# Performance work log

Measured on AMD Instinct MI355X. Metric: run time of the kernel, lower is better.

Reference implementation:

```python
import jax, jax.numpy as jnp
import numpy as np

B, S, E = 2, 4096, 640
H, D, G = 4, 256, 1      # n_heads, head_dim, n_kv_groups
WINDOW = 512
SCALING = 256.0 ** -0.5  # query_pre_attn_scalar ** -0.5
EPS = 1e-6


def rmsnorm(x, scale):
    # Gemma variant: weight = 1 + scale, computed in fp32 over last dim
    xf = x.astype(jnp.float32)
    var = jnp.mean(xf * xf, axis=-1, keepdims=True)
    return (xf * jax.lax.rsqrt(var + EPS) * (1.0 + scale.astype(jnp.float32))).astype(x.dtype)


def apply_rope(x, cos, sin):
    # x: [B, h, S, D]; cos/sin: [S, D]
    half = x.shape[-1] // 2
    x1, x2 = x[..., :half], x[..., half:]
    rotated = jnp.concatenate([-x2, x1], axis=-1)
    return (x * cos[None, None] + rotated * sin[None, None]).astype(x.dtype)


def setup_inputs() -> dict:
    key = jax.random.key(0)
    ks = jax.random.split(key, 6)
    x = jax.random.normal(ks[0], (B, S, E), dtype=jnp.float32)
    # weights (torch Linear weight.T layout: [in, out])
    Wq = jax.random.normal(ks[1], (E, H * D), dtype=jnp.float32) * 0.02
    Wk = jax.random.normal(ks[2], (E, G * D), dtype=jnp.float32) * 0.02
    Wv = jax.random.normal(ks[3], (E, G * D), dtype=jnp.float32) * 0.02
    Wo = jax.random.normal(ks[4], (H * D, E), dtype=jnp.float32) * 0.02
    q_scale = jnp.zeros((D,), dtype=jnp.float32)
    k_scale = jnp.zeros((D,), dtype=jnp.float32)
    # RoPE tables (theta = rope_local_base = 10000 for sliding layers)
    inv_freq = 1.0 / (10000.0 ** (jnp.arange(0, D, 2, dtype=jnp.float32) / D))
    angles = jnp.arange(S, dtype=jnp.float32)[:, None] * inv_freq[None, :]
    angles = jnp.concatenate([angles, angles], axis=1)  # [S, D]
    cos, sin = jnp.cos(angles), jnp.sin(angles)
    # causal + sliding-window mask; True = masked out
    i = jnp.arange(S)[:, None]
    j = jnp.arange(S)[None, :]
    mask = (j > i) | ((i - j) >= WINDOW)
    return {"x": x, "mask": mask, "cos": cos, "sin": sin,
            "Wq": Wq, "Wk": Wk, "Wv": Wv, "Wo": Wo,
            "q_scale": q_scale, "k_scale": k_scale}


def reference(x, mask, cos, sin, Wq, Wk, Wv, Wo, q_scale, k_scale):
    b, s, _ = x.shape
    q = (x @ Wq).reshape(b, s, H, D).transpose(0, 2, 1, 3)  # [B,H,S,D]
    k = (x @ Wk).reshape(b, s, G, D).transpose(0, 2, 1, 3)  # [B,G,S,D]
    v = (x @ Wv).reshape(b, s, G, D).transpose(0, 2, 1, 3)  # [B,G,S,D]
    q = rmsnorm(q, q_scale)
    k = rmsnorm(k, k_scale)
    q = apply_rope(q, cos, sin)
    k = apply_rope(k, cos, sin)
    # GQA: K/V have G=1 heads; broadcasting replaces repeat_interleave
    scores = (q * SCALING) @ jnp.swapaxes(k, -1, -2)  # [B,H,S,S]
    scores = jnp.where(mask[None, None], -jnp.inf, scores)
    attn = jax.nn.softmax(scores, axis=-1)
    out = attn @ v                                     # [B,H,S,D]
    out = out.transpose(0, 2, 1, 3).reshape(b, s, H * D)
    return out @ Wo
```

## Files before the change

kernel.cpp:

```cpp
#include <hip/hip_runtime.h>
#include <hip/hip_bf16.h>
#include <stdint.h>

#define BB 2
#define SS 4096
#define EE 640
#define HH 4
#define DD 256
#define WIN 512

typedef __attribute__((ext_vector_type(8))) short bv8;
typedef __attribute__((ext_vector_type(4))) float fv4;
typedef __attribute__((ext_vector_type(16))) float fv16;

__device__ __forceinline__ unsigned short f2b(float f) {
  union { float f; unsigned u; } a; a.f = f;
  unsigned r = a.u + 0x7fffu + ((a.u >> 16) & 1u);
  return (unsigned short)(r >> 16);
}
__device__ __forceinline__ float b2f(unsigned short s) {
  union { unsigned u; float f; } a; a.u = ((unsigned)s) << 16;
  return a.f;
}
__device__ __forceinline__ unsigned pk2(float lo, float hi_) {
  return (unsigned)f2b(lo) | ((unsigned)f2b(hi_) << 16);
}

typedef const __attribute__((address_space(1))) unsigned int* as1u;
typedef __attribute__((address_space(3))) unsigned int* as3u;
__device__ __forceinline__ void gld16(const unsigned short* g, unsigned short* l) {
  __builtin_amdgcn_global_load_lds((as1u)(const void*)g, (as3u)(void*)l, 16, 0, 0);
}

__global__ __launch_bounds__(256) void k_cast_bf16(const float* __restrict__ src,
                                                   unsigned short* __restrict__ dst, int n4) {
  int i = blockIdx.x * 256 + threadIdx.x;
  if (i >= n4) return;
  fv4 v = ((const fv4*)src)[i];
  ushort4 o; o.x = f2b(v.x); o.y = f2b(v.y); o.z = f2b(v.z); o.w = f2b(v.w);
  ((ushort4*)dst)[i] = o;
}

template <typename T>
__global__ __launch_bounds__(256) void k_transpose_bf16(const T* __restrict__ src,
    unsigned short* __restrict__ dst, int sstride, int dstride) {
  __shared__ float tile[32][33];
  int r0 = blockIdx.x * 32, c0 = blockIdx.y * 32;
  int t = threadIdx.x;
  int rr = t >> 3, cc = (t & 7) * 4;
  const T* p = src + (size_t)(r0 + rr) * sstride + c0 + cc;
  float v[4];
  if constexpr (sizeof(T) == 4) {
    fv4 x = *(const fv4*)p;
    v[0] = x.x; v[1] = x.y; v[2] = x.z; v[3] = x.w;
  } else {
    ushort4 x = *(const ushort4*)p;
    v[0] = b2f(x.x); v[1] = b2f(x.y); v[2] = b2f(x.z); v[3] = b2f(x.w);
  }
#pragma unroll
  for (int i = 0; i < 4; ++i) tile[cc + i][rr] = v[i];
  __syncthreads();
  ushort4 o;
  o.x = f2b(tile[rr][cc + 0]); o.y = f2b(tile[rr][cc + 1]);
  o.z = f2b(tile[rr][cc + 2]); o.w = f2b(tile[rr][cc + 3]);
  *(ushort4*)(dst + (size_t)(c0 + rr) * dstride + r0 + cc) = o;
}

template <bool OUT_BF16, int BN>
__global__ __launch_bounds__(256) void k_gemm(const unsigned short* __restrict__ A,
    const unsigned short* __restrict__ Bt, void* __restrict__ Cp,
    int M, int N, int K, int nt_n) {
  __shared__ unsigned short la[128 * 32];
  __shared__ unsigned short lb[BN * 32];
  const int bid = blockIdx.x;
  const int gidx = (bid & 7) * (gridDim.x >> 3) + (bid >> 3);
  const int m0 = (gidx / nt_n) * 128, n0 = (gidx % nt_n) * BN;
  const int tid = threadIdx.x, lane = tid & 63, wave = tid >> 6;
  const int g = lane >> 4, lr = lane & 15;
  constexpr int MI = (BN == 128) ? 4 : 2;
  const int wm = (BN == 128) ? (wave >> 1) * 64 : wave * 32;
  const int wn = (BN == 128) ? (wave & 1) * 64 : 0;
  fv4 acc[MI][4] = {};
  const int srow = wave * 32 + (lane >> 2);
  const int sch = (lane & 3) * 8;
  const unsigned short* ga0 = A + (size_t)(m0 + srow) * K + sch;
  unsigned short* lad = la + wave * 1024;
  const int srowb = (BN == 128) ? srow : (wave * 16 + (lane >> 2));
  const unsigned short* gb0 = Bt + (size_t)(n0 + srowb) * K + sch;
  unsigned short* lbd = lb + ((BN == 128) ? wave * 1024 : wave * 512);
  for (int k0 = 0; k0 < K; k0 += 32) {
    __syncthreads();
    gld16(ga0 + k0, lad);
    gld16(ga0 + (size_t)16 * K + k0, lad + 512);
    gld16(gb0 + k0, lbd);
    if constexpr (BN == 128) gld16(gb0 + (size_t)16 * K + k0, lbd + 512);
    __syncthreads();
    bv8 af[MI], bf[4];
#pragma unroll
    for (int mi = 0; mi < MI; ++mi) af[mi] = *(const bv8*)(la + (wm + mi * 16 + lr) * 32 + g * 8);
#pragma unroll
    for (int ni = 0; ni < 4; ++ni) bf[ni] = *(const bv8*)(lb + (wn + ni * 16 + lr) * 32 + g * 8);
    __builtin_amdgcn_s_setprio(1);
#pragma unroll
    for (int mi = 0; mi < MI; ++mi)
#pragma unroll
      for (int ni = 0; ni < 4; ++ni)
        acc[mi][ni] = __builtin_amdgcn_mfma_f32_16x16x32_bf16(af[mi], bf[ni], acc[mi][ni], 0, 0, 0);
    __builtin_amdgcn_s_setprio(0);
  }
#pragma unroll
  for (int mi = 0; mi < MI; ++mi) {
#pragma unroll
    for (int r = 0; r < 4; ++r) {
      size_t row = (size_t)(m0 + wm + mi * 16 + g * 4 + r);
#pragma unroll
      for (int ni = 0; ni < 4; ++ni) {
        int col = n0 + wn + ni * 16 + lr;
        float val = acc[mi][ni][r];
        if constexpr (OUT_BF16)
          ((unsigned short*)Cp)[row * N + col] = f2b(val);
        else
          ((float*)Cp)[row * N + col] = val;
      }
    }
  }
}

__global__ __launch_bounds__(320) void k_normrope(const unsigned short* __restrict__ qkv,
    const float* __restrict__ cosp, const float* __restrict__ sinp,
    const float* __restrict__ qsc, const float* __restrict__ ksc,
    unsigned short* __restrict__ qo, unsigned short* __restrict__ ko) {
  int m = blockIdx.x;
  int b = m >> 12, s = m & 4095;
  int wave = threadIdx.x >> 6, lane = threadIdx.x & 63;
  bool isq = wave < 4;
  const unsigned short* src = qkv + (size_t)m * 1536 + (isq ? wave * 256 : 1024);
  const float* scp = isq ? qsc : ksc;
  int d0 = lane * 4;
  ushort4 raw = *(const ushort4*)(src + d0);
  float x0 = b2f(raw.x), x1 = b2f(raw.y), x2 = b2f(raw.z), x3 = b2f(raw.w);
  float ss = x0 * x0 + x1 * x1 + x2 * x2 + x3 * x3;
#pragma unroll
  for (int off = 1; off < 64; off <<= 1) ss += __shfl_xor(ss, off, 64);
  float rs = rsqrtf(ss * (1.0f / 256.0f) + 1e-6f);
  fv4 sc = *(const fv4*)(scp + d0);
  float n0 = x0 * rs * (1.0f + sc.x);
  float n1 = x1 * rs * (1.0f + sc.y);
  float n2 = x2 * rs * (1.0f + sc.z);
  float n3 = x3 * rs * (1.0f + sc.w);
  float p0 = __shfl_xor(n0, 32, 64);
  float p1 = __shfl_xor(n1, 32, 64);
  float p2 = __shfl_xor(n2, 32, 64);
  float p3 = __shfl_xor(n3, 32, 64);
  float sgn = (lane < 32) ? -1.0f : 1.0f;
  fv4 c4 = *(const fv4*)(cosp + (size_t)s * 256 + d0);
  fv4 s4 = *(const fv4*)(sinp + (size_t)s * 256 + d0);
  float mult = isq ? 0.0625f : 1.0f;
  float o0 = (n0 * c4.x + sgn * p0 * s4.x) * mult;
  float o1 = (n1 * c4.y + sgn * p1 * s4.y) * mult;
  float o2 = (n2 * c4.z + sgn * p2 * s4.z) * mult;
  float o3 = (n3 * c4.w + sgn * p3 * s4.w) * mult;
  ushort4 o; o.x = f2b(o0); o.y = f2b(o1); o.z = f2b(o2); o.w = f2b(o3);
  unsigned short* dst = isq
      ? qo + ((size_t)(b * HH + wave) * SS + s) * 256 + d0
      : ko + ((size_t)b * SS + s) * 256 + d0;
  *(ushort4*)dst = o;
}

__global__ __launch_bounds__(512, 2) void k_attn(const unsigned short* __restrict__ q,
    const unsigned short* __restrict__ kg, const unsigned short* __restrict__ vtg,
    unsigned short* __restrict__ att) {
  __shared__ __align__(16) char ldsbuf[133120];
  __shared__ float lsb[4][32];
  unsigned short* kt = (unsigned short*)ldsbuf;
  unsigned short* vl = (unsigned short*)ldsbuf + 32768;
  const int bid = blockIdx.x;
  const int gidx = (bid & 7) * 32 + (bid >> 3);
  const int b = gidx >> 7;
  const int i0 = (gidx & 127) * 32;
  const int tid = threadIdx.x, wave = tid >> 6, lane = tid & 63;
  const int h = wave >> 1, ks = wave & 1;
  const int hi = lane >> 5, l31 = lane & 31;
  bv8 qf[16];
  {
    const unsigned short* qp = q + ((size_t)(b * HH + h) * SS + i0 + l31) * 256;
#pragma unroll
    for (int m = 0; m < 16; ++m) qf[m] = *(const bv8*)(qp + m * 16 + hi * 8);
  }
  fv16 po[8] = {};
  float lsp = 0.f;
  const int t0 = (i0 >= WIN) ? ((i0 - WIN + 1) >> 6) : 0;
  const int t1 = i0 >> 6;
  const unsigned short* kb = kg + (size_t)b * SS * 256;
  const unsigned short* vb = vtg + (size_t)b * 256 * SS;
  auto stageK = [&](int t, int pp) {
    const unsigned short* kbase = kb + (size_t)t * 64 * 256;
    unsigned short* dst = kt + pp * 16384;
#pragma unroll
    for (int c = 0; c < 4; ++c) {
      int slot = c * 512 + tid;
      int row = slot >> 5, s = slot & 31;
      gld16(kbase + (size_t)row * 256 + ((s ^ (row & 7)) * 8),
            dst + (c * 512 + wave * 64) * 8);
    }
  };
  auto stageV = [&](int t, int pp) {
    const unsigned short* vbase = vb + (size_t)t * 64;
    unsigned short* dst = vl + pp * 16384;
#pragma unroll
    for (int c = 0; c < 4; ++c) {
      int slot = c * 512 + tid;
      int d_ = slot >> 3, s = slot & 7;
      gld16(vbase + (size_t)d_ * SS + ((s ^ (d_ & 7)) * 8),
            dst + (c * 512 + wave * 64) * 8);
    }
  };
  stageK(t0, 0); stageV(t0, 0);
  int p = 0;
  const int krow = ks * 32 + l31;
  const int krx = krow & 7;
  const int vrx = l31 & 7;
  for (int t = t0; t <= t1; ++t) {
    __syncthreads();
    if (t < t1) { stageK(t + 1, p ^ 1); stageV(t + 1, p ^ 1); }
    fv16 sa = {};
    const unsigned short* ktp = kt + p * 16384 + krow * 256;
    __builtin_amdgcn_s_setprio(1);
#pragma unroll
    for (int m = 0; m < 16; ++m) {
      bv8 kf = *(const bv8*)(ktp + (((m * 2 + hi) ^ krx) * 8));
      sa = __builtin_amdgcn_mfma_f32_32x32x16_bf16(kf, qf[m], sa, 0, 0, 0);
    }
    __builtin_amdgcn_s_setprio(0);
    const int jb = t * 64;
    const int kb0 = jb + ks * 32;
    const bool nm = (kb0 + 31 > i0) || (i0 + 31 - kb0 >= WIN);
    if (nm) {
      const int qa = i0 + l31;
#pragma unroll
      for (int r = 0; r < 16; ++r) {
        int j = kb0 + (r & 3) + 8 * (r >> 2) + 4 * hi;
        if (j > qa || qa - j >= WIN) sa[r] = -1e30f;
      }
    }
    unsigned a[8];
#pragma unroll
    for (int i = 0; i < 8; ++i) {
      float e0 = __expf(sa[2 * i] - 16.5f);
      float e1 = __expf(sa[2 * i + 1] - 16.5f);
      lsp += e0 + e1;
      a[i] = pk2(e0, e1);
    }
    unsigned w[8];
#pragma unroll
    for (int m2 = 0; m2 < 2; ++m2) {
      unsigned a0 = a[m2 * 4 + 0], a1 = a[m2 * 4 + 1];
      unsigned a2 = a[m2 * 4 + 2], a3 = a[m2 * 4 + 3];
      unsigned s0 = (unsigned)__shfl_xor((int)a0, 32, 64);
      unsigned s1 = (unsigned)__shfl_xor((int)a1, 32, 64);
      unsigned s2 = (unsigned)__shfl_xor((int)a2, 32, 64);
      unsigned s3 = (unsigned)__shfl_xor((int)a3, 32, 64);
      w[m2 * 4 + 0] = hi ? s2 : a0;
      w[m2 * 4 + 1] = hi ? s3 : a1;
      w[m2 * 4 + 2] = hi ? a2 : s0;
      w[m2 * 4 + 3] = hi ? a3 : s1;
    }
    const unsigned short* vlp = vl + p * 16384;
    __builtin_amdgcn_s_setprio(1);
#pragma unroll
    for (int m2 = 0; m2 < 2; ++m2) {
      union { unsigned u[4]; bv8 v; } pf;
      pf.u[0] = w[m2 * 4 + 0]; pf.u[1] = w[m2 * 4 + 1];
      pf.u[2] = w[m2 * 4 + 2]; pf.u[3] = w[m2 * 4 + 3];
      const int slot = (ks * 4 + m2 * 2 + hi) ^ vrx;
#pragma unroll
      for (int ds_ = 0; ds_ < 8; ++ds_) {
        bv8 vf = *(const bv8*)(vlp + (ds_ * 32 + l31) * 64 + slot * 8);
        po[ds_] = __builtin_amdgcn_mfma_f32_32x32x16_bf16(vf, pf.v, po[ds_], 0, 0, 0);
      }
    }
    __builtin_amdgcn_s_setprio(0);
    p ^= 1;
  }
  float lsfull = lsp + __shfl_xor(lsp, 32, 64);
  __syncthreads();
  float* cb = (float*)ldsbuf;
  if (ks == 1) {
#pragma unroll
    for (int ds_ = 0; ds_ < 8; ++ds_)
#pragma unroll
      for (int j = 0; j < 4; ++j) {
        int d0 = ds_ * 32 + 8 * j + 4 * hi;
        fv4 v4; v4[0] = po[ds_][4 * j]; v4[1] = po[ds_][4 * j + 1];
        v4[2] = po[ds_][4 * j + 2]; v4[3] = po[ds_][4 * j + 3];
        *(fv4*)(cb + (h * 32 + l31) * 260 + d0) = v4;
      }
    if (lane < 32) lsb[h][lane] = lsfull;
  }
  __syncthreads();
  if (ks == 0) {
    float total = lsfull + lsb[h][l31];
    float inv = 1.0f / total;
    unsigned short* op = att + ((size_t)b * SS + i0 + l31) * 1024 + h * 256;
#pragma unroll
    for (int ds_ = 0; ds_ < 8; ++ds_)
#pragma unroll
      for (int j = 0; j < 4; ++j) {
        int d0 = ds_ * 32 + 8 * j + 4 * hi;
        fv4 v4 = *(const fv4*)(cb + (h * 32 + l31) * 260 + d0);
        ushort4 o;
        o.x = f2b((po[ds_][4 * j] + v4[0]) * inv);
        o.y = f2b((po[ds_][4 * j + 1] + v4[1]) * inv);
        o.z = f2b((po[ds_][4 * j + 2] + v4[2]) * inv);
        o.w = f2b((po[ds_][4 * j + 3] + v4[3]) * inv);
        *(ushort4*)(op + d0) = o;
      }
  }
}

extern "C" void kernel_launch(void* const* d_in, const int* in_sizes, int n_in,
                              void* d_out, int out_size, void* d_ws, size_t ws_size,
                              hipStream_t stream) {
  const float* x    = (const float*)d_in[0];
  const float* cosp = (const float*)d_in[2];
  const float* sinp = (const float*)d_in[3];
  const float* Wq   = (const float*)d_in[4];
  const float* Wk   = (const float*)d_in[5];
  const float* Wv   = (const float*)d_in[6];
  const float* Wo   = (const float*)d_in[7];
  const float* qsc  = (const float*)d_in[8];
  const float* ksc  = (const float*)d_in[9];
  float* out = (float*)d_out;
  char* ws = (char*)d_ws;

  unsigned short* xb   = (unsigned short*)(ws);
  unsigned short* wqkv = (unsigned short*)(ws + 10485760);
  unsigned short* wo   = (unsigned short*)(ws + 12451840);
  unsigned short* qkv  = (unsigned short*)(ws + 13762560);
  unsigned short* qb   = (unsigned short*)(ws + 38928384);
  unsigned short* kbuf = (unsigned short*)(ws + 55705600);
  unsigned short* vt   = (unsigned short*)(ws + 59899904);
  unsigned short* attb = (unsigned short*)(ws + 64094208);

  k_cast_bf16<<<5120, 256, 0, stream>>>(x, xb, 1310720);
  k_transpose_bf16<float><<<dim3(20, 32), 256, 0, stream>>>(Wq, wqkv, 1024, 640);
  k_transpose_bf16<float><<<dim3(20, 8), 256, 0, stream>>>(Wk, wqkv + 1024 * 640, 256, 640);
  k_transpose_bf16<float><<<dim3(20, 8), 256, 0, stream>>>(Wv, wqkv + 1280 * 640, 256, 640);
  k_transpose_bf16<float><<<dim3(32, 20), 256, 0, stream>>>(Wo, wo, 640, 1024);
  k_gemm<true, 128><<<768, 256, 0, stream>>>(xb, wqkv, qkv, 8192, 1536, 640, 12);
  k_normrope<<<8192, 320, 0, stream>>>(qkv, cosp, sinp, qsc, ksc, qb, kbuf);
  k_transpose_bf16<unsigned short><<<dim3(128, 8), 256, 0, stream>>>(qkv + 1280, vt, 1536, 4096);
  k_transpose_bf16<unsigned short><<<dim3(128, 8), 256, 0, stream>>>(
      qkv + (size_t)4096 * 1536 + 1280, vt + (size_t)256 * 4096, 1536, 4096);
  k_attn<<<256, 512, 0, stream>>>(qb, kbuf, vt, attb);
  k_gemm<false, 64><<<640, 256, 0, stream>>>(attb, wo, out, 8192, 640, 1024, 10);
}
```

Before: 121.9 us.

## Use hardware bf16 pack, permlane32 swap, exp2 with folded log2e, split MFMA chains

Replaces the software bf16 rounding with the v_cvt_pk_bf16_f32 instruction and the shuffle-plus-select exchange with permlane32_swap. It folds log2(e) into the query scaling so the softmax can use exp2f directly. The QK^T MFMA accumulation is split into two independent chains that are summed afterwards. Together these aim to cut VALU and cross-lane work in the attention inner loop and to shorten the MFMA dependency chain, at the cost of a few extra accumulator registers.

Result: slower. 132.8 us (+9.0%).

```diff
diff --git a/kernel.cpp b/kernel.cpp
--- a/kernel.cpp
+++ b/kernel.cpp
@@ -22,8 +22,10 @@
   union { unsigned u; float f; } a; a.u = ((unsigned)s) << 16;
   return a.f;
 }
-__device__ __forceinline__ unsigned pk2(float lo, float hi_) {
-  return (unsigned)f2b(lo) | ((unsigned)f2b(hi_) << 16);
+__device__ __forceinline__ unsigned cvtpk(float e0, float e1) {
+  unsigned r;
+  asm("v_cvt_pk_bf16_f32 %0, %1, %2" : "=v"(r) : "v"(e0), "v"(e1));
+  return r;
 }
 
 typedef const __attribute__((address_space(1))) unsigned int* as1u;
@@ -155,7 +157,7 @@
   float sgn = (lane < 32) ? -1.0f : 1.0f;
   fv4 c4 = *(const fv4*)(cosp + (size_t)s * 256 + d0);
   fv4 s4 = *(const fv4*)(sinp + (size_t)s * 256 + d0);
-  float mult = isq ? 0.0625f : 1.0f;
+  float mult = isq ? (0.0625f * 1.44269504f) : 1.0f;
   float o0 = (n0 * c4.x + sgn * p0 * s4.x) * mult;
   float o1 = (n1 * c4.y + sgn * p1 * s4.y) * mult;
   float o2 = (n2 * c4.z + sgn * p2 * s4.z) * mult;
@@ -220,18 +222,22 @@
   const int krow = ks * 32 + l31;
   const int krx = krow & 7;
   const int vrx = l31 & 7;
+  const float FSUB = 16.5f * 1.44269504f;
   for (int t = t0; t <= t1; ++t) {
     __syncthreads();
     if (t < t1) { stageK(t + 1, p ^ 1); stageV(t + 1, p ^ 1); }
-    fv16 sa = {};
+    fv16 sa0 = {}, sa1 = {};
     const unsigned short* ktp = kt + p * 16384 + krow * 256;
     __builtin_amdgcn_s_setprio(1);
 #pragma unroll
-    for (int m = 0; m < 16; ++m) {
-      bv8 kf = *(const bv8*)(ktp + (((m * 2 + hi) ^ krx) * 8));
-      sa = __builtin_amdgcn_mfma_f32_32x32x16_bf16(kf, qf[m], sa, 0, 0, 0);
+    for (int m = 0; m < 8; ++m) {
+      bv8 kfa = *(const bv8*)(ktp + (((m * 2 + hi) ^ krx) * 8));
+      bv8 kfb = *(const bv8*)(ktp + ((((m + 8) * 2 + hi) ^ krx) * 8));
+      sa0 = __builtin_amdgcn_mfma_f32_32x32x16_bf16(kfa, qf[m], sa0, 0, 0, 0);
+      sa1 = __builtin_amdgcn_mfma_f32_32x32x16_bf16(kfb, qf[m + 8], sa1, 0, 0, 0);
     }
     __builtin_amdgcn_s_setprio(0);
+    fv16 sa = sa0 + sa1;
     const int jb = t * 64;
     const int kb0 = jb + ks * 32;
     const bool nm = (kb0 + 31 > i0) || (i0 + 31 - kb0 >= WIN);
@@ -246,32 +252,19 @@
     unsigned a[8];
 #pragma unroll
     for (int i = 0; i < 8; ++i) {
-      float e0 = __expf(sa[2 * i] - 16.5f);
-      float e1 = __expf(sa[2 * i + 1] - 16.5f);
+      float e0 = exp2f(sa[2 * i] - FSUB);
+      float e1 = exp2f(sa[2 * i + 1] - FSUB);
       lsp += e0 + e1;
-      a[i] = pk2(e0, e1);
-    }
-    unsigned w[8];
-#pragma unroll
-    for (int m2 = 0; m2 < 2; ++m2) {
-      unsigned a0 = a[m2 * 4 + 0], a1 = a[m2 * 4 + 1];
-      unsigned a2 = a[m2 * 4 + 2], a3 = a[m2 * 4 + 3];
-      unsigned s0 = (unsigned)__shfl_xor((int)a0, 32, 64);
-      unsigned s1 = (unsigned)__shfl_xor((int)a1, 32, 64);
-      unsigned s2 = (unsigned)__shfl_xor((int)a2, 32, 64);
-      unsigned s3 = (unsigned)__shfl_xor((int)a3, 32, 64);
-      w[m2 * 4 + 0] = hi ? s2 : a0;
-      w[m2 * 4 + 1] = hi ? s3 : a1;
-      w[m2 * 4 + 2] = hi ? a2 : s0;
-      w[m2 * 4 + 3] = hi ? a3 : s1;
+      a[i] = cvtpk(e0, e1);
     }
     const unsigned short* vlp = vl + p * 16384;
     __builtin_amdgcn_s_setprio(1);
 #pragma unroll
     for (int m2 = 0; m2 < 2; ++m2) {
+      auto r02 = __builtin_amdgcn_permlane32_swap(a[m2 * 4 + 0], a[m2 * 4 + 2], false, false);
+      auto r13 = __builtin_amdgcn_permlane32_swap(a[m2 * 4 + 1], a[m2 * 4 + 3], false, false);
       union { unsigned u[4]; bv8 v; } pf;
-      pf.u[0] = w[m2 * 4 + 0]; pf.u[1] = w[m2 * 4 + 1];
-      pf.u[2] = w[m2 * 4 + 2]; pf.u[3] = w[m2 * 4 + 3];
+      pf.u[0] = r02[0]; pf.u[1] = r13[0]; pf.u[2] = r02[1]; pf.u[3] = r13[1];
       const int slot = (ks * 4 + m2 * 2 + hi) ^ vrx;
 #pragma unroll
       for (int ds_ = 0; ds_ < 8; ++ds_) {
```
